# Kernel tuning notes

Measured on AMD Instinct MI355X. Metric: run time of the kernel, lower is better.

## Reference

```python
import itertools
import jax, jax.numpy as jnp
import numpy as np

N_FIELDS = 8
N_NS = 4          # fields 0..3 are non-sequence, fields 4..7 are sequence
DIM_NS = 100000   # vocab of non-sequence fields
DIM_SEQ = 1000    # vocab of sequence fields
SEQ_LEN = 50
D = 64            # emb_dim
B = 16384
N_SLOTS = N_FIELDS - 1  # tables per field (one per ordered perm partner)
PAIRS = list(itertools.combinations(range(N_FIELDS), 2))


def setup_inputs() -> dict:
    key = jax.random.key(0)
    k1, k2, k3, k4 = jax.random.split(key, 4)
    # one table per ordered perm (i, j): stored as tables_*[i_local * N_SLOTS + slot(j)]
    tables_ns = jax.random.normal(k1, (N_NS * N_SLOTS, DIM_NS, D), jnp.float32) * 0.01
    tables_seq = jax.random.normal(k2, (N_NS * N_SLOTS, DIM_SEQ, D), jnp.float32) * 0.01
    idx_ns = jax.random.randint(k3, (N_NS, B, 1), 0, DIM_NS)
    idx_seq = jax.random.randint(k4, (N_NS, B, SEQ_LEN), 0, DIM_SEQ)
    return {"tables_ns": tables_ns, "tables_seq": tables_seq,
            "idx_ns": idx_ns, "idx_seq": idx_seq}


def _embed(field, other, tables_ns, tables_seq, idx_ns, idx_seq):
    """Embedding for perm table 'field-other', mean-pooled over sequence -> [B, D]."""
    slot = other if other < field else other - 1
    if field < N_NS:  # non-sequence: inputs [B, 1] -> [B, D]
        return tables_ns[field * N_SLOTS + slot][idx_ns[field, :, 0]]
    # sequence: inputs [B, L] -> gather [B, L, D] -> mean over L
    e = tables_seq[(field - N_NS) * N_SLOTS + slot][idx_seq[field - N_NS]]
    return e.mean(axis=1)


def reference(tables_ns, tables_seq, idx_ns, idx_seq):
    # sum over all field pairs of <emb_{a-b}(x_a), emb_{b-a}(x_b)>  -> [B, 1]
    total = jnp.zeros((B, 1), dtype=tables_ns.dtype)
    for a, b in PAIRS:
        ea = _embed(a, b, tables_ns, tables_seq, idx_ns, idx_seq)
        eb = _embed(b, a, tables_ns, tables_seq, idx_ns, idx_seq)
        total = total + jnp.sum(ea * eb, axis=-1, keepdims=True)
    return total
```

## Files before the change

### kernel.cpp

```cpp
#include <hip/hip_runtime.h>

#define NF 8
#define NNS 4
#define NSL 7
#define DIM_NS 100000
#define DIM_SEQ 1000
#define SEQ_LEN 50
#define DD 64
#define BB 16384
#define SCALE 4096.0f

typedef unsigned int u32;
typedef float floatx2 __attribute__((ext_vector_type(2)));

__global__ __launch_bounds__(256) void pack_seq_kernel(const float* __restrict__ tseq,
                                                       uint2* __restrict__ packed) {
  int fv = blockIdx.x * 4 + (threadIdx.x >> 6);
  int d  = threadIdx.x & 63;
  int f = fv / DIM_SEQ, v = fv - f * DIM_SEQ;
  float h[8];
#pragma unroll
  for (int s = 0; s < NSL; ++s) {
    h[s] = tseq[((size_t)((f * NSL + s) * DIM_SEQ + v)) * DD + d] * SCALE;
  }
  h[7] = 0.f;
  u32 lo = __builtin_amdgcn_cvt_pk_fp8_f32(h[0], h[1], 0, false);
  lo     = __builtin_amdgcn_cvt_pk_fp8_f32(h[2], h[3], lo, true);
  u32 hi = __builtin_amdgcn_cvt_pk_fp8_f32(h[4], h[5], 0, false);
  hi     = __builtin_amdgcn_cvt_pk_fp8_f32(h[6], h[7], hi, true);
  uint2 val; val.x = lo; val.y = hi;
  packed[(size_t)fv * DD + d] = val;
}

__device__ __constant__ int PAIR_A[28] = {0,0,0,0,0,0,0, 1,1,1,1,1,1, 2,2,2,2,2, 3,3,3,3, 4,4,4, 5,5, 6};
__device__ __constant__ int PAIR_C[28] = {1,2,3,4,5,6,7, 2,3,4,5,6,7, 3,4,5,6,7, 4,5,6,7, 5,6,7, 6,7, 7};

template <bool PACKED>
__global__ __launch_bounds__(256, 4) void ffm_kernel(const float* __restrict__ tns,
                                                     const float* __restrict__ tseq,
                                                     const uint2* __restrict__ packed,
                                                     const int* __restrict__ idx_ns,
                                                     const int* __restrict__ idx_seq,
                                                     float* __restrict__ out) {
  __shared__ float e_lds[NF * NSL * DD];
  __shared__ float partial[4];

  const int lane = threadIdx.x & 63;
  const int w    = threadIdx.x >> 6;
  const int b    = blockIdx.x;
  const int d    = lane;

  float ns[NSL];
  {
    const int ia = idx_ns[w * BB + b];
#pragma unroll
    for (int s = 0; s < NSL; ++s) {
      ns[s] = tns[((size_t)(w * NSL + s) * DIM_NS + ia) * DD + d];
    }
  }

  int myidx = 0;
  if (lane < SEQ_LEN) myidx = idx_seq[(w * BB + b) * SEQ_LEN + lane];

  if (PACKED) {
    const int half = lane >> 5;
    const int m    = lane & 31;
    const char* tb = (const char*)packed + ((size_t)w * DIM_SEQ) * 512 + m * 16;

    floatx2 aA0 = {0.f, 0.f}, aA1 = aA0, aA2 = aA0, aA3 = aA0;
    floatx2 aB0 = aA0, aB1 = aA0, aB2 = aA0, aB3 = aA0;
#pragma unroll 5
    for (int k = 0; k < SEQ_LEN / 2; ++k) {
      const int i0 = __builtin_amdgcn_readlane(myidx, 2 * k);
      const int i1 = __builtin_amdgcn_readlane(myidx, 2 * k + 1);
      const int iv = half ? i1 : i0;
      const uint4 u = *reinterpret_cast<const uint4*>(tb + (size_t)iv * 512);
      aA0 += __builtin_amdgcn_cvt_pk_f32_fp8(u.x, false);
      aA1 += __builtin_amdgcn_cvt_pk_f32_fp8(u.x, true);
      aA2 += __builtin_amdgcn_cvt_pk_f32_fp8(u.y, false);
      aA3 += __builtin_amdgcn_cvt_pk_f32_fp8(u.y, true);
      aB0 += __builtin_amdgcn_cvt_pk_f32_fp8(u.z, false);
      aB1 += __builtin_amdgcn_cvt_pk_f32_fp8(u.z, true);
      aB2 += __builtin_amdgcn_cvt_pk_f32_fp8(u.w, false);
      aB3 += __builtin_amdgcn_cvt_pk_f32_fp8(u.w, true);
    }

    float sA[NSL] = {aA0.x, aA0.y, aA1.x, aA1.y, aA2.x, aA2.y, aA3.x};
    float sB[NSL] = {aB0.x, aB0.y, aB1.x, aB1.y, aB2.x, aB2.y, aB3.x};
    const float inv = 1.0f / (50.0f * SCALE);
#pragma unroll
    for (int s = 0; s < NSL; ++s) {
      const float tA = (sA[s] + __shfl_xor(sA[s], 32)) * inv;
      const float tB = (sB[s] + __shfl_xor(sB[s], 32)) * inv;
      if (half == 0) {
        float2 v2; v2.x = tA; v2.y = tB;
        *reinterpret_cast<float2*>(&e_lds[((NNS + w) * NSL + s) * DD + 2 * m]) = v2;
      }
    }
  } else {
    float acc[NSL];
#pragma unroll
    for (int s = 0; s < NSL; ++s) acc[s] = 0.f;
#pragma unroll 5
    for (int l = 0; l < SEQ_LEN; ++l) {
      const int iv = __builtin_amdgcn_readlane(myidx, l);
#pragma unroll
      for (int s = 0; s < NSL; ++s) {
        acc[s] += tseq[((size_t)(w * NSL + s) * DIM_SEQ + iv) * DD + d];
      }
    }
#pragma unroll
    for (int s = 0; s < NSL; ++s)
      e_lds[((NNS + w) * NSL + s) * DD + d] = acc[s] * (1.0f / 50.0f);
  }

#pragma unroll
  for (int s = 0; s < NSL; ++s) e_lds[(w * NSL + s) * DD + d] = ns[s];

  __syncthreads();

  float r = 0.f;
#pragma unroll
  for (int p = 0; p < NSL; ++p) {
    const int pi = w * NSL + p;
    const int a  = PAIR_A[pi];
    const int c  = PAIR_C[pi];
    r += e_lds[(a * NSL + (c - 1)) * DD + d] * e_lds[(c * NSL + a) * DD + d];
  }

#pragma unroll
  for (int off = 32; off > 0; off >>= 1) r += __shfl_down(r, off);
  if (lane == 0) partial[w] = r;
  __syncthreads();
  if (threadIdx.x == 0) out[b] = partial[0] + partial[1] + partial[2] + partial[3];
}

extern "C" void kernel_launch(void* const* d_in, const int* in_sizes, int n_in,
                              void* d_out, int out_size, void* d_ws, size_t ws_size,
                              hipStream_t stream) {
  const float* tns    = (const float*)d_in[0];
  const float* tseq   = (const float*)d_in[1];
  const int*   idx_ns = (const int*)d_in[2];
  const int*   idx_sq = (const int*)d_in[3];
  float* out = (float*)d_out;

  const size_t packed_bytes = (size_t)NNS * DIM_SEQ * DD * 8;
  if (ws_size >= packed_bytes) {
    pack_seq_kernel<<<NNS * DIM_SEQ / 4, 256, 0, stream>>>(tseq, (uint2*)d_ws);
    ffm_kernel<true><<<BB, 256, 0, stream>>>(tns, tseq, (const uint2*)d_ws,
                                             idx_ns, idx_sq, out);
  } else {
    ffm_kernel<false><<<BB, 256, 0, stream>>>(tns, tseq, nullptr,
                                              idx_ns, idx_sq, out);
  }
}
```

Before: 113.0 us.

## Pool sequence embeddings from LDS-resident fp8 table chunks in separate kernel

Splits the work into three kernels. The first repacks the sequence tables into per-(field, slot-pair) fp8 chunks. The second loads each 128KB chunk into LDS and mean-pools the sequence gathers from shared memory, writing bf16 pooled embeddings to a workspace buffer. The third does the non-sequence gathers and the pairwise dot products. The aim is to turn the random global gathers of sequence rows into LDS reads. In exchange it adds a roughly 58MB intermediate write and read, two extra launches, and bf16 rounding on top of the fp8 quantization.

```diff
diff --git a/kernel.cpp b/kernel.cpp
--- a/kernel.cpp
+++ b/kernel.cpp
@@ -9,9 +9,124 @@
 #define DD 64
 #define BB 16384
 #define SCALE 4096.0f
+#define NBLK 32
+#define BBLK (BB / NBLK)
 
 typedef unsigned int u32;
+typedef unsigned short u16;
 typedef float floatx2 __attribute__((ext_vector_type(2)));
+
+__device__ __forceinline__ u16 f2bf(float x) {
+  u32 u = __float_as_uint(x);
+  return (u16)((u + 0x7FFFu + ((u >> 16) & 1u)) >> 16);
+}
+
+__global__ __launch_bounds__(256) void pack2_kernel(const float* __restrict__ tseq,
+                                                    u32* __restrict__ packed2) {
+  const int id = blockIdx.x * 256 + threadIdx.x;
+  const int m = id & 31;
+  const int v = (id >> 5) % DIM_SEQ;
+  const int fsg = id / (32 * DIM_SEQ);
+  const int f = fsg >> 2, sg = fsg & 3;
+  const int s0 = 2 * sg, s1 = 2 * sg + 1;
+  float a = tseq[((size_t)(f * NSL + s0) * DIM_SEQ + v) * DD + 2 * m] * SCALE;
+  float b = tseq[((size_t)(f * NSL + s0) * DIM_SEQ + v) * DD + 2 * m + 1] * SCALE;
+  float c = 0.f, d2 = 0.f;
+  if (s1 < NSL) {
+    c  = tseq[((size_t)(f * NSL + s1) * DIM_SEQ + v) * DD + 2 * m] * SCALE;
+    d2 = tseq[((size_t)(f * NSL + s1) * DIM_SEQ + v) * DD + 2 * m + 1] * SCALE;
+  }
+  u32 r = __builtin_amdgcn_cvt_pk_fp8_f32(a, b, 0, false);
+  r     = __builtin_amdgcn_cvt_pk_fp8_f32(c, d2, r, true);
+  packed2[id] = r;
+}
+
+__global__ __launch_bounds__(1024) void pool_kernel(const u32* __restrict__ packed2,
+                                                    const int* __restrict__ idx_seq,
+                                                    u32* __restrict__ Ebuf) {
+  __shared__ u32 chunk[32 * DIM_SEQ];
+  const int fsg = blockIdx.x & 15, nb = blockIdx.x >> 4;
+  const int f = fsg >> 2, sg = fsg & 3;
+
+  const u32* src = packed2 + (size_t)fsg * 32 * DIM_SEQ;
+  for (int i = threadIdx.x; i < 32 * DIM_SEQ; i += 1024) chunk[i] = src[i];
+  __syncthreads();
+
+  const int W = threadIdx.x >> 6, lane = threadIdx.x & 63;
+  const int half = lane >> 5, m = lane & 31;
+  const float inv = 1.0f / (50.0f * SCALE);
+  const int s = half ? (2 * sg + 1) : (2 * sg);
+
+  for (int e = 0; e < BBLK / 16; ++e) {
+    const int b = __builtin_amdgcn_readfirstlane(nb * BBLK + W * 32 + e);
+    const int* __restrict__ ip = idx_seq + ((size_t)f * BB + b) * SEQ_LEN;
+    floatx2 acc0 = {0.f, 0.f}, acc1 = {0.f, 0.f};
+#pragma unroll
+    for (int k = 0; k < SEQ_LEN / 2; ++k) {
+      const int i0 = ip[2 * k];
+      const int i1 = ip[2 * k + 1];
+      const int v = half ? i1 : i0;
+      const u32 u = chunk[v * 32 + m];
+      acc0 += __builtin_amdgcn_cvt_pk_f32_fp8(u, false);
+      acc1 += __builtin_amdgcn_cvt_pk_f32_fp8(u, true);
+    }
+    acc0.x += __shfl_xor(acc0.x, 32); acc0.y += __shfl_xor(acc0.y, 32);
+    acc1.x += __shfl_xor(acc1.x, 32); acc1.y += __shfl_xor(acc1.y, 32);
+    const floatx2 w2 = half ? acc1 : acc0;
+    if (s < NSL) {
+      const u32 outw = (u32)f2bf(w2.x * inv) | ((u32)f2bf(w2.y * inv) << 16);
+      Ebuf[((size_t)b * 28 + f * NSL + s) * 32 + m] = outw;
+    }
+  }
+}
+
+__device__ __constant__ int PAIR_A[28] = {0,0,0,0,0,0,0, 1,1,1,1,1,1, 2,2,2,2,2, 3,3,3,3, 4,4,4, 5,5, 6};
+__device__ __constant__ int PAIR_C[28] = {1,2,3,4,5,6,7, 2,3,4,5,6,7, 3,4,5,6,7, 4,5,6,7, 5,6,7, 6,7, 7};
+
+__global__ __launch_bounds__(256, 4) void dot_kernel(const float* __restrict__ tns,
+                                                     const u32* __restrict__ Ebuf,
+                                                     const int* __restrict__ idx_ns,
+                                                     float* __restrict__ out) {
+  __shared__ float e_lds[NF * NSL * DD];
+  __shared__ float partial[4];
+  const int lane = threadIdx.x & 63;
+  const int w    = threadIdx.x >> 6;
+  const int b    = blockIdx.x;
+  const int d    = lane;
+
+  float ns[NSL];
+  {
+    const int ia = idx_ns[w * BB + b];
+#pragma unroll
+    for (int sIt = 0; sIt < NSL; ++sIt) {
+      ns[sIt] = tns[((size_t)(w * NSL + sIt) * DIM_NS + ia) * DD + d];
+    }
+  }
+  const u16* Eh = (const u16*)Ebuf;
+#pragma unroll
+  for (int sIt = 0; sIt < NSL; ++sIt) {
+    const u32 raw = Eh[((size_t)b * 28 + w * NSL + sIt) * DD + d];
+    e_lds[((NNS + w) * NSL + sIt) * DD + d] = __uint_as_float(raw << 16);
+  }
+#pragma unroll
+  for (int sIt = 0; sIt < NSL; ++sIt) e_lds[(w * NSL + sIt) * DD + d] = ns[sIt];
+
+  __syncthreads();
+
+  float r = 0.f;
+#pragma unroll
+  for (int p = 0; p < NSL; ++p) {
+    const int pi = w * NSL + p;
+    const int a = PAIR_A[pi];
+    const int c = PAIR_C[pi];
+    r += e_lds[(a * NSL + (c - 1)) * DD + d] * e_lds[(c * NSL + a) * DD + d];
+  }
+#pragma unroll
+  for (int off = 32; off > 0; off >>= 1) r += __shfl_down(r, off);
+  if (lane == 0) partial[w] = r;
+  __syncthreads();
+  if (threadIdx.x == 0) out[b] = partial[0] + partial[1] + partial[2] + partial[3];
+}
 
 __global__ __launch_bounds__(256) void pack_seq_kernel(const float* __restrict__ tseq,
                                                        uint2* __restrict__ packed) {
@@ -31,9 +146,6 @@
   uint2 val; val.x = lo; val.y = hi;
   packed[(size_t)fv * DD + d] = val;
 }
-
-__device__ __constant__ int PAIR_A[28] = {0,0,0,0,0,0,0, 1,1,1,1,1,1, 2,2,2,2,2, 3,3,3,3, 4,4,4, 5,5, 6};
-__device__ __constant__ int PAIR_C[28] = {1,2,3,4,5,6,7, 2,3,4,5,6,7, 3,4,5,6,7, 4,5,6,7, 5,6,7, 6,7, 7};
 
 template <bool PACKED>
 __global__ __launch_bounds__(256, 4) void ffm_kernel(const float* __restrict__ tns,
@@ -44,7 +156,6 @@
                                                      float* __restrict__ out) {
   __shared__ float e_lds[NF * NSL * DD];
   __shared__ float partial[4];
-
   const int lane = threadIdx.x & 63;
   const int w    = threadIdx.x >> 6;
   const int b    = blockIdx.x;
@@ -58,7 +169,6 @@
       ns[s] = tns[((size_t)(w * NSL + s) * DIM_NS + ia) * DD + d];
     }
   }
-
   int myidx = 0;
   if (lane < SEQ_LEN) myidx = idx_seq[(w * BB + b) * SEQ_LEN + lane];
 
@@ -66,7 +176,6 @@
     const int half = lane >> 5;
     const int m    = lane & 31;
     const char* tb = (const char*)packed + ((size_t)w * DIM_SEQ) * 512 + m * 16;
-
     floatx2 aA0 = {0.f, 0.f}, aA1 = aA0, aA2 = aA0, aA3 = aA0;
     floatx2 aB0 = aA0, aB1 = aA0, aB2 = aA0, aB3 = aA0;
 #pragma unroll 5
@@ -84,7 +193,6 @@
       aB2 += __builtin_amdgcn_cvt_pk_f32_fp8(u.w, false);
       aB3 += __builtin_amdgcn_cvt_pk_f32_fp8(u.w, true);
     }
-
     float sA[NSL] = {aA0.x, aA0.y, aA1.x, aA1.y, aA2.x, aA2.y, aA3.x};
     float sB[NSL] = {aB0.x, aB0.y, aB1.x, aB1.y, aB2.x, aB2.y, aB3.x};
     const float inv = 1.0f / (50.0f * SCALE);
@@ -116,18 +224,16 @@
 
 #pragma unroll
   for (int s = 0; s < NSL; ++s) e_lds[(w * NSL + s) * DD + d] = ns[s];
-
   __syncthreads();
 
   float r = 0.f;
 #pragma unroll
   for (int p = 0; p < NSL; ++p) {
     const int pi = w * NSL + p;
-    const int a  = PAIR_A[pi];
-    const int c  = PAIR_C[pi];
+    const int a = PAIR_A[pi];
+    const int c = PAIR_C[pi];
     r += e_lds[(a * NSL + (c - 1)) * DD + d] * e_lds[(c * NSL + a) * DD + d];
   }
-
 #pragma unroll
   for (int off = 32; off > 0; off >>= 1) r += __shfl_down(r, off);
   if (lane == 0) partial[w] = r;
@@ -144,8 +250,17 @@
   const int*   idx_sq = (const int*)d_in[3];
   float* out = (float*)d_out;
 
-  const size_t packed_bytes = (size_t)NNS * DIM_SEQ * DD * 8;
-  if (ws_size >= packed_bytes) {
+  const size_t packed2_bytes = (size_t)16 * 32 * DIM_SEQ * 4;
+  const size_t E_bytes       = (size_t)BB * 28 * DD * 2;
+  const size_t tier1_bytes   = packed2_bytes + E_bytes;
+
+  if (ws_size >= tier1_bytes) {
+    u32* packed2 = (u32*)d_ws;
+    u32* Ebuf    = (u32*)((char*)d_ws + packed2_bytes);
+    pack2_kernel<<<512000 / 256, 256, 0, stream>>>(tseq, packed2);
+    pool_kernel<<<16 * NBLK, 1024, 0, stream>>>(packed2, idx_sq, Ebuf);
+    dot_kernel<<<BB, 256, 0, stream>>>(tns, Ebuf, idx_ns, out);
+  } else if (ws_size >= packed2_bytes) {
     pack_seq_kernel<<<NNS * DIM_SEQ / 4, 256, 0, stream>>>(tseq, (uint2*)d_ws);
     ffm_kernel<true><<<BB, 256, 0, stream>>>(tns, tseq, (const uint2*)d_ws,
                                              idx_ns, idx_sq, out);
```

Measured after the change: 178.4 us. 1.58x slower.
